# Kernel optimization log

Hardware: AMD Instinct MI355X
Metric: run time of the kernel (lower is better)

Reference implementation:

```python
import jax, jax.numpy as jnp
import numpy as np

B = 8192
FEATURE_NUM = 200      # categorical fields
NUMERIC_SIZE = 100     # dense features
FEATURE_SIZE = 1_000_000  # vocab for one-hot weights
EMBED = 64
OUT_DIM = 1


def setup_inputs() -> dict:
    key = jax.random.key(0)
    k_idx, k_num, k_w1, k_w2, k_v1, k_v2 = jax.random.split(key, 6)
    # first FEATURE_NUM columns are categorical indices stored as floats
    idx = jax.random.randint(k_idx, (B, FEATURE_NUM), 0, FEATURE_SIZE).astype(jnp.float32)
    numeric = jax.random.normal(k_num, (B, NUMERIC_SIZE), dtype=jnp.float32)
    inputs = jnp.concatenate([idx, numeric], axis=1)  # [B, 300]
    scale = 0.05
    return {
        "inputs": inputs,
        "w_one_hot": jax.random.normal(k_w1, (FEATURE_SIZE, OUT_DIM), dtype=jnp.float32) * scale,
        "w_numeric": jax.random.normal(k_w2, (NUMERIC_SIZE, OUT_DIM), dtype=jnp.float32) * scale,
        "v_one_hot": jax.random.normal(k_v1, (FEATURE_SIZE, EMBED), dtype=jnp.float32) * scale,
        "v_numeric": jax.random.normal(k_v2, (NUMERIC_SIZE, EMBED), dtype=jnp.float32) * scale,
        "b": jnp.zeros((OUT_DIM,), dtype=jnp.float32),
    }


def reference(inputs, w_one_hot, w_numeric, v_one_hot, v_numeric, b):
    # split categorical indices / numeric features
    idx = inputs[:, :FEATURE_NUM].astype(jnp.int32)   # [B, F]
    numeric = inputs[:, FEATURE_NUM:]                 # [B, N]

    # first order: gathered scalar weights (output_dim==1) + linear on numeric
    first_order = jnp.sum(w_one_hot[idx, 0], axis=1) + jnp.sum(numeric @ w_numeric, axis=1)  # [B]

    # second order FM: 0.5 * sum_e ((sum_f v)^2 - sum_f v^2) over concatenated fields
    sec_w = v_one_hot[idx]                            # [B, F, E] gathered embeddings
    num_w = numeric[:, :, None] * v_numeric[None]     # [B, N, E]
    field_sum = jnp.sum(sec_w, axis=1) + jnp.sum(num_w, axis=1)            # [B, E]
    field_sq_sum = jnp.sum(sec_w * sec_w, axis=1) + jnp.sum(num_w * num_w, axis=1)  # [B, E]
    second_order = 0.5 * jnp.sum(field_sum * field_sum - field_sq_sum, axis=1)      # [B]

    out = first_order + second_order + b[0]
    return out[:, None]  # [B, 1]
```

## Files before the change

kernel.cpp:

```cpp
#include <hip/hip_runtime.h>

#define BATCH 8192
#define FEATURE_NUM 200
#define NUMERIC_SIZE 100
#define IN_STRIDE (FEATURE_NUM + NUMERIC_SIZE)
#define EMBED 64
#define WAVES_PER_BLOCK 4
#define CHUNK 8


__device__ __forceinline__ void load8(const float* __restrict__ v_one_hot,
                                      const int* sidx, int c, int lane,
                                      float vv[CHUNK]) {
    #pragma unroll
    for (int s = 0; s < CHUNK; ++s) {
        int idx = sidx[c + s];
        vv[s] = v_one_hot[idx * EMBED + lane];
    }
}

__device__ __forceinline__ void accum8(const float vv[CHUNK],
                                       float& fs, float& fss) {
    #pragma unroll
    for (int s = 0; s < CHUNK; ++s) { fs += vv[s]; fss += vv[s] * vv[s]; }
}

__global__ __launch_bounds__(256, 8) void fm_layer_kernel(
    const float* __restrict__ inputs,
    const float* __restrict__ w_one_hot,
    const float* __restrict__ w_numeric,
    const float* __restrict__ v_one_hot,
    const float* __restrict__ v_numeric,
    const float* __restrict__ bias,
    float* __restrict__ out)
{
    __shared__ int   s_idx[WAVES_PER_BLOCK][FEATURE_NUM];
    __shared__ float s_num[WAVES_PER_BLOCK][NUMERIC_SIZE];

    const int lane = threadIdx.x & 63;
    const int wave = threadIdx.x >> 6;
    const int row  = blockIdx.x * WAVES_PER_BLOCK + wave;

    const float* in_row = inputs + (size_t)row * IN_STRIDE;

    for (int j = lane; j < IN_STRIDE; j += 64) {
        float x = in_row[j];
        if (j < FEATURE_NUM) s_idx[wave][j] = (int)x;
        else                 s_num[wave][j - FEATURE_NUM] = x;
    }
    __syncthreads();

    const int* sidx = s_idx[wave];
    const float* snum = s_num[wave];

    float w0 = w_one_hot[sidx[lane]];
    float w1 = w_one_hot[sidx[lane + 64]];
    float w2 = w_one_hot[sidx[lane + 128]];
    float w3 = w_one_hot[sidx[192 + (lane & 7)]];

    float fs = 0.f, fss = 0.f;

    float va[CHUNK], vb[CHUNK];
    load8(v_one_hot, sidx, 0, lane, va);

    #pragma unroll 1
    for (int j = 0; j < NUMERIC_SIZE; j += 10) {
        #pragma unroll
        for (int s = 0; s < 10; ++s) {
            float x  = snum[j + s];
            float v  = v_numeric[(j + s) * EMBED + lane];
            float nv = x * v;
            fs += nv; fss += nv * nv;
        }
    }

    #pragma unroll 1
    for (int k = 0; k < 12; ++k) {
        load8(v_one_hot, sidx, (2 * k + 1) * CHUNK, lane, vb);
        accum8(va, fs, fss);
        load8(v_one_hot, sidx, (2 * k + 2) * CHUNK, lane, va);
        accum8(vb, fs, fss);
    }
    accum8(va, fs, fss);

    float first = w0 + w1 + w2 + ((lane < 8) ? w3 : 0.f);
    first += snum[lane] * w_numeric[lane];
    if (lane < NUMERIC_SIZE - 64) first += snum[lane + 64] * w_numeric[lane + 64];

    float partial = first + 0.5f * (fs * fs - fss);

    #pragma unroll
    for (int off = 32; off > 0; off >>= 1)
        partial += __shfl_down(partial, off, 64);

    if (lane == 0) out[row] = partial + bias[0];
}

extern "C" void kernel_launch(void* const* d_in, const int* in_sizes, int n_in,
                              void* d_out, int out_size, void* d_ws, size_t ws_size,
                              hipStream_t stream) {
    const float* inputs    = (const float*)d_in[0];
    const float* w_one_hot = (const float*)d_in[1];
    const float* w_numeric = (const float*)d_in[2];
    const float* v_one_hot = (const float*)d_in[3];
    const float* v_numeric = (const float*)d_in[4];
    const float* bias      = (const float*)d_in[5];
    float* out = (float*)d_out;

    dim3 grid(BATCH / WAVES_PER_BLOCK);
    dim3 block(256);
    fm_layer_kernel<<<grid, block, 0, stream>>>(
        inputs, w_one_hot, w_numeric, v_one_hot, v_numeric, bias, out);
}
```

Baseline: 369.5 us.

## Gather embeddings with float4 loads across four lane groups and triple buffering

Each wave is split into four 16-lane groups. Each group reads a different embedding row, and each lane loads a float4 of four embedding components, so one instruction fetches four rows per wave instead of one. Accumulation uses four partial sums per lane, combined across groups with xor shuffles before the square-and-subtract step. The software pipeline goes from double to triple buffering, and the numeric part uses the same float4 layout. This cuts the number of load instructions and raises memory-level parallelism for the random row gathers, at the cost of more registers and extra shuffle reductions.

```diff
diff --git a/kernel.cpp b/kernel.cpp
--- a/kernel.cpp
+++ b/kernel.cpp
@@ -6,24 +6,24 @@
 #define IN_STRIDE (FEATURE_NUM + NUMERIC_SIZE)
 #define EMBED 64
 #define WAVES_PER_BLOCK 4
-#define CHUNK 8
 
 
-__device__ __forceinline__ void load8(const float* __restrict__ v_one_hot,
-                                      const int* sidx, int c, int lane,
-                                      float vv[CHUNK]) {
-    #pragma unroll
-    for (int s = 0; s < CHUNK; ++s) {
-        int idx = sidx[c + s];
-        vv[s] = v_one_hot[idx * EMBED + lane];
-    }
-}
+#define LOADC(B0, B1, c) do {                                              \
+    int2 ff = *(const int2*)(sidx + 8*(c) + 2*g);                          \
+    B0 = *(const float4*)(v_one_hot + (unsigned)ff.x * 64u + sub4);        \
+    B1 = *(const float4*)(v_one_hot + (unsigned)ff.y * 64u + sub4);        \
+} while (0)
 
-__device__ __forceinline__ void accum8(const float vv[CHUNK],
-                                       float& fs, float& fss) {
-    #pragma unroll
-    for (int s = 0; s < CHUNK; ++s) { fs += vv[s]; fss += vv[s] * vv[s]; }
-}
+#define ACCUM(B0, B1) do {                                                 \
+    fs0 += B0.x; fss0 += B0.x * B0.x;                                      \
+    fs1 += B0.y; fss1 += B0.y * B0.y;                                      \
+    fs2 += B0.z; fss2 += B0.z * B0.z;                                      \
+    fs3 += B0.w; fss3 += B0.w * B0.w;                                      \
+    fs0 += B1.x; fss0 += B1.x * B1.x;                                      \
+    fs1 += B1.y; fss1 += B1.y * B1.y;                                      \
+    fs2 += B1.z; fss2 += B1.z * B1.z;                                      \
+    fs3 += B1.w; fss3 += B1.w * B1.w;                                      \
+} while (0)
 
 __global__ __launch_bounds__(256, 8) void fm_layer_kernel(
     const float* __restrict__ inputs,
@@ -40,6 +40,8 @@
     const int lane = threadIdx.x & 63;
     const int wave = threadIdx.x >> 6;
     const int row  = blockIdx.x * WAVES_PER_BLOCK + wave;
+    const int g    = lane >> 4;
+    const unsigned sub4 = (unsigned)(lane & 15) * 4u;
 
     const float* in_row = inputs + (size_t)row * IN_STRIDE;
 
@@ -58,36 +60,49 @@
     float w2 = w_one_hot[sidx[lane + 128]];
     float w3 = w_one_hot[sidx[192 + (lane & 7)]];
 
-    float fs = 0.f, fss = 0.f;
+    float fs0 = 0.f, fs1 = 0.f, fs2 = 0.f, fs3 = 0.f;
+    float fss0 = 0.f, fss1 = 0.f, fss2 = 0.f, fss3 = 0.f;
 
-    float va[CHUNK], vb[CHUNK];
-    load8(v_one_hot, sidx, 0, lane, va);
+    float4 va0, va1, vb0, vb1, vc0, vc1;
 
-    #pragma unroll 1
-    for (int j = 0; j < NUMERIC_SIZE; j += 10) {
-        #pragma unroll
-        for (int s = 0; s < 10; ++s) {
-            float x  = snum[j + s];
-            float v  = v_numeric[(j + s) * EMBED + lane];
-            float nv = x * v;
-            fs += nv; fss += nv * nv;
-        }
+    LOADC(va0, va1, 0);
+    LOADC(vb0, vb1, 1);
+
+    #pragma unroll 5
+    for (int t = 0; t < 25; ++t) {
+        int f = 4 * t + g;
+        float x = snum[f];
+        float4 v = *(const float4*)(v_numeric + (unsigned)f * 64u + sub4);
+        float n0 = x * v.x; fs0 += n0; fss0 += n0 * n0;
+        float n1 = x * v.y; fs1 += n1; fss1 += n1 * n1;
+        float n2 = x * v.z; fs2 += n2; fss2 += n2 * n2;
+        float n3 = x * v.w; fs3 += n3; fss3 += n3 * n3;
     }
 
     #pragma unroll 1
-    for (int k = 0; k < 12; ++k) {
-        load8(v_one_hot, sidx, (2 * k + 1) * CHUNK, lane, vb);
-        accum8(va, fs, fss);
-        load8(v_one_hot, sidx, (2 * k + 2) * CHUNK, lane, va);
-        accum8(vb, fs, fss);
+    for (int t = 0; t < 7; ++t) {
+        int c = 3 * t;
+        LOADC(vc0, vc1, c + 2); ACCUM(va0, va1);
+        LOADC(va0, va1, c + 3); ACCUM(vb0, vb1);
+        LOADC(vb0, vb1, c + 4); ACCUM(vc0, vc1);
     }
-    accum8(va, fs, fss);
+    LOADC(vc0, vc1, 23); ACCUM(va0, va1);
+    LOADC(va0, va1, 24); ACCUM(vb0, vb1);
+    ACCUM(vc0, vc1);
+    ACCUM(va0, va1);
+
+    #define XRED(v) v += __shfl_xor(v, 16, 64); v += __shfl_xor(v, 32, 64)
+    XRED(fs0); XRED(fs1); XRED(fs2); XRED(fs3);
+    XRED(fss0); XRED(fss1); XRED(fss2); XRED(fss3);
+    #undef XRED
 
     float first = w0 + w1 + w2 + ((lane < 8) ? w3 : 0.f);
     first += snum[lane] * w_numeric[lane];
     if (lane < NUMERIC_SIZE - 64) first += snum[lane + 64] * w_numeric[lane + 64];
 
-    float partial = first + 0.5f * (fs * fs - fss);
+    float so = (fs0 * fs0 - fss0) + (fs1 * fs1 - fss1)
+             + (fs2 * fs2 - fss2) + (fs3 * fs3 - fss3);
+    float partial = first + ((g == 0) ? 0.5f * so : 0.f);
 
     #pragma unroll
     for (int off = 32; off > 0; off >>= 1)
```

Result: no change. 367.1 us (-0.7%).
